# Kernel optimization log

Hardware: AMD Instinct MI355X
Metric: run time of the kernel (lower is better)

The kernel has to match this reference:

```python
import jax, jax.numpy as jnp
import numpy as np

LN_EPS = 1e-5
NEG_INF = -1e38


def wkv_scan(w, u, k, v):
    """Numerically-stable RWKV WKV recurrence (matches wkv_cuda forward).
    w: [C] (negative decay), u: [C] bonus, k/v: [B,T,C]. Returns y: [B,T,C]."""
    Bdim, T, C = k.shape

    def step(carry, kv_t):
        p, q, o = carry  # running num, den, log-scale, each [B,C]
        kt, vt = kv_t
        no = jnp.maximum(o, u + kt)
        A = jnp.exp(o - no)
        Bw = jnp.exp(u + kt - no)
        y = (A * p + Bw * vt) / (A * q + Bw)
        no2 = jnp.maximum(w + o, kt)
        A2 = jnp.exp(w + o - no2)
        B2 = jnp.exp(kt - no2)
        return (A2 * p + B2 * vt, A2 * q + B2, no2), y

    init = (jnp.zeros((Bdim, C), k.dtype), jnp.zeros((Bdim, C), k.dtype),
            jnp.full((Bdim, C), NEG_INF, k.dtype))
    kT = jnp.moveaxis(k, 1, 0)  # [T,B,C]
    vT = jnp.moveaxis(v, 1, 0)
    _, ys = jax.lax.scan(step, init, (kT, vT))
    return jnp.moveaxis(ys, 0, 1)  # [B,T,C]


def setup_inputs() -> dict:
    key = jax.random.key(0)
    ks = jax.random.split(key, 8)
    B, C, H, W = 16, 192, 56, 56
    s = 0.02
    x = jax.random.normal(ks[0], (B, C, H, W), jnp.float32)
    Wk = jax.random.normal(ks[1], (C, C), jnp.float32) * s
    Wv = jax.random.normal(ks[2], (C, C), jnp.float32) * s
    Wr = jax.random.normal(ks[3], (C, C), jnp.float32) * s
    Wo = jax.random.normal(ks[4], (C, C), jnp.float32) * s
    ln_g = jnp.ones((C,), jnp.float32)
    ln_b = jnp.zeros((C,), jnp.float32)
    w_decay = -6.0 + 0.1 * jax.random.normal(ks[5], (C,), jnp.float32)
    u = 0.1 * jax.random.normal(ks[6], (C,), jnp.float32)
    return {"x": x, "Wk": Wk, "Wv": Wv, "Wr": Wr, "Wo": Wo,
            "ln_g": ln_g, "ln_b": ln_b, "w_decay": w_decay, "u": u}


def reference(x, Wk, Wv, Wr, Wo, ln_g, ln_b, w_decay, u):
    B, C, H, W = x.shape
    xs = jnp.transpose(x.reshape(B, C, H * W), (0, 2, 1))  # [B,T,C]
    k = jnp.einsum('btc,dc->btd', xs, Wk)
    v = jnp.einsum('btc,dc->btd', xs, Wv)
    r = jnp.einsum('btc,dc->btd', xs, Wr)
    real_w = -jnp.exp(w_decay)
    x_fwd = wkv_scan(real_w, u, k, v)
    x_bwd = jnp.flip(wkv_scan(real_w, u, jnp.flip(k, 1), jnp.flip(v, 1)), 1)
    x_bi = 0.5 * (x_fwd + x_bwd)
    h = jax.nn.sigmoid(r) * x_bi
    mu = jnp.mean(h, axis=-1, keepdims=True)
    var = jnp.var(h, axis=-1, keepdims=True)
    h = (h - mu) * jax.lax.rsqrt(var + LN_EPS) * ln_g + ln_b
    out = jnp.einsum('btc,dc->btd', h, Wo)  # dropout is identity at eval
    return jnp.transpose(out, (0, 2, 1)).reshape(B, C, H, W)
```

## Files before the change

### kernel.cpp

```cpp
#include <hip/hip_runtime.h>

#define BB 16
#define CC 192
#define TPIX 3136
#define NCH 49
#define CHL 64
#define NNELE ((size_t)BB * TPIX * CC)
#define NSTATE ((size_t)2 * BB * NCH * CC)
#define WCH (CC * CC)

typedef __attribute__((ext_vector_type(8))) short bf16x8;
typedef __attribute__((ext_vector_type(4))) short bf16x4;
typedef __attribute__((ext_vector_type(4))) float f32x4;
typedef __attribute__((ext_vector_type(16))) float f32x16;

__device__ __forceinline__ unsigned short f2bf(float f) {
    union { float f; unsigned u; } v; v.f = f;
    unsigned r = v.u + 0x7FFFu + ((v.u >> 16) & 1u);
    return (unsigned short)(r >> 16);
}
__device__ __forceinline__ float bf2f(unsigned short h) {
    union { unsigned u; float f; } v; v.u = ((unsigned)h) << 16;
    return v.f;
}


__global__ __launch_bounds__(256) void wcvt_frag(
    const float* __restrict__ Wk, const float* __restrict__ Wv,
    const float* __restrict__ Wr, const float* __restrict__ Wo,
    unsigned short* __restrict__ wfrag)
{
    const int id = blockIdx.x * 256 + threadIdx.x;
    const int m = id / 4608;
    const int r = id % 4608;
    const int tile = r >> 6;
    const int lane = r & 63;
    const int dr = tile / 12, tk = tile % 12;
    const int d = dr * 32 + (lane & 31);
    const int c = tk * 16 + (lane >> 5) * 8;
    const float* W = (m == 0) ? Wk : (m == 1) ? Wv : (m == 2) ? Wr : Wo;
    const float4 a = *(const float4*)&W[d * CC + c];
    const float4 b = *(const float4*)&W[d * CC + c + 4];
    bf16x8 o;
    o[0] = (short)f2bf(a.x); o[1] = (short)f2bf(a.y);
    o[2] = (short)f2bf(a.z); o[3] = (short)f2bf(a.w);
    o[4] = (short)f2bf(b.x); o[5] = (short)f2bf(b.y);
    o[6] = (short)f2bf(b.z); o[7] = (short)f2bf(b.w);
    *(bf16x8*)&wfrag[(size_t)m * WCH + (size_t)tile * 512 + lane * 8] = o;
}

__global__ __launch_bounds__(256) void xcvt_frag(
    const float* __restrict__ x, unsigned short* __restrict__ xfrag)
{
    const int t0 = blockIdx.x * 32;
    const int b  = blockIdx.y;
    __shared__ float ls[CC][33];
    const int tid = threadIdx.x;
#pragma unroll
    for (int it = 0; it < 6; ++it) {
        const int c  = it * 32 + (tid >> 3);
        const int t4 = (tid & 7) * 4;
        *(float4*)&ls[c][t4] =
            *(const float4*)&x[((size_t)b * CC + c) * TPIX + t0 + t4];
    }
    __syncthreads();
    const size_t tbase = ((size_t)(b * TPIX + t0) >> 5) * 12;
#pragma unroll
    for (int it = 0; it < 3; ++it) {
        const int id = it * 256 + tid;
        const int tk = id >> 6;
        const int lane = id & 63;
        const int r32 = lane & 31;
        const int c0 = tk * 16 + (lane >> 5) * 8;
        bf16x8 o;
#pragma unroll
        for (int e = 0; e < 8; ++e)
            o[e] = (short)f2bf(ls[c0 + e][r32]);
        *(bf16x8*)&xfrag[(tbase + tk) * 512 + lane * 8] = o;
    }
}

__global__ __launch_bounds__(512) void proj_mfma32(
    const unsigned short* __restrict__ xfrag,
    const unsigned short* __restrict__ wfrag,
    unsigned short* __restrict__ kbf, unsigned short* __restrict__ vbf,
    unsigned short* __restrict__ rbf)
{
    __shared__ unsigned short wlds[WCH];
    const int tid  = threadIdx.x;
    const int lane = tid & 63;
    const int wv   = tid >> 6;
    const int tw   = wv >> 1;
    const int dwav = wv & 1;
    const int l31  = lane & 31;
    const int kh   = lane >> 5;
    const int m    = blockIdx.z;

    const unsigned short* wm = wfrag + (size_t)m * WCH;
#pragma unroll
    for (int it = 0; it < 9; ++it) {
        const int off = (it * 512 + tid) * 8;
        *(bf16x8*)&wlds[off] = *(const bf16x8*)&wm[off];
    }
    __syncthreads();

    const size_t row0 = (size_t)blockIdx.x * 128 + tw * 32;
    const size_t xtb  = (row0 >> 5) * 12;

    f32x16 acc[3];
#pragma unroll
    for (int nn = 0; nn < 3; ++nn)
#pragma unroll
        for (int e = 0; e < 16; ++e) acc[nn][e] = 0.f;

    bf16x8 xf = *(const bf16x8*)&xfrag[xtb * 512 + lane * 8];
#pragma unroll
    for (int ks = 0; ks < 12; ++ks) {
        bf16x8 nxf;
        if (ks < 11)
            nxf = *(const bf16x8*)&xfrag[(xtb + ks + 1) * 512 + lane * 8];
        bf16x8 wf[3];
#pragma unroll
        for (int nn = 0; nn < 3; ++nn)
            wf[nn] = *(const bf16x8*)&wlds[((dwav * 3 + nn) * 12 + ks) * 512 + lane * 8];
#pragma unroll
        for (int nn = 0; nn < 3; ++nn)
            acc[nn] = __builtin_amdgcn_mfma_f32_32x32x16_bf16(
                xf, wf[nn], acc[nn], 0, 0, 0);
        if (ks < 11) xf = nxf;
    }

    unsigned short* om = (m == 0) ? kbf : (m == 1) ? vbf : rbf;
#pragma unroll
    for (int nn = 0; nn < 3; ++nn) {
        const int d = dwav * 96 + nn * 32 + l31;
#pragma unroll
        for (int q = 0; q < 16; ++q) {
            const int t = (q & 3) + 8 * (q >> 2) + 4 * kh;
            om[(row0 + t) * CC + d] = f2bf(acc[nn][q]);
        }
    }
}

__global__ __launch_bounds__(512) void outproj_mfma32(
    const unsigned short* __restrict__ hfrag,
    const unsigned short* __restrict__ wo,
    float* __restrict__ out)
{
    __shared__ unsigned short wlds[WCH];
    const int tid  = threadIdx.x;
    const int lane = tid & 63;
    const int wv   = tid >> 6;
    const int tw   = wv >> 1;
    const int dwav = wv & 1;
    const int l31  = lane & 31;
    const int kh   = lane >> 5;

#pragma unroll
    for (int it = 0; it < 9; ++it) {
        const int off = (it * 512 + tid) * 8;
        *(bf16x8*)&wlds[off] = *(const bf16x8*)&wo[off];
    }
    __syncthreads();

    const size_t row0 = (size_t)blockIdx.x * 128 + tw * 32;
    const size_t htb  = (row0 >> 5) * 12;

    f32x16 acc[3];
#pragma unroll
    for (int nn = 0; nn < 3; ++nn)
#pragma unroll
        for (int e = 0; e < 16; ++e) acc[nn][e] = 0.f;

    bf16x8 hf = *(const bf16x8*)&hfrag[htb * 512 + lane * 8];
#pragma unroll
    for (int ks = 0; ks < 12; ++ks) {
        bf16x8 nhf;
        if (ks < 11)
            nhf = *(const bf16x8*)&hfrag[(htb + ks + 1) * 512 + lane * 8];
        bf16x8 wf[3];
#pragma unroll
        for (int nn = 0; nn < 3; ++nn)
            wf[nn] = *(const bf16x8*)&wlds[((dwav * 3 + nn) * 12 + ks) * 512 + lane * 8];
#pragma unroll
        for (int nn = 0; nn < 3; ++nn)
            acc[nn] = __builtin_amdgcn_mfma_f32_32x32x16_bf16(
                hf, wf[nn], acc[nn], 0, 0, 0);
        if (ks < 11) hf = nhf;
    }

#pragma unroll
    for (int nn = 0; nn < 3; ++nn) {
        const int d = dwav * 96 + nn * 32 + l31;
#pragma unroll
        for (int q2 = 0; q2 < 4; ++q2) {
            const size_t grow = row0 + 4 * kh + 8 * q2;
            const int b  = (int)(grow / TPIX);
            const int tl = (int)(grow % TPIX);
            f32x4 v4 = {acc[nn][q2 * 4 + 0], acc[nn][q2 * 4 + 1],
                        acc[nn][q2 * 4 + 2], acc[nn][q2 * 4 + 3]};
            *(f32x4*)&out[((size_t)b * CC + d) * TPIX + tl] = v4;
        }
    }
}

__global__ __launch_bounds__(256) void wkv_chunk_kernel(
    const unsigned short* __restrict__ kb, const unsigned short* __restrict__ vb,
    const float* __restrict__ wdec,
    float* __restrict__ sp, float* __restrict__ sq, float* __restrict__ so)
{
    const int gid = blockIdx.x * 256 + threadIdx.x;
    const int c  = gid % CC;
    const int r  = gid / CC;
    const int ch = r % NCH;
    const int r2 = r / NCH;
    const int b  = r2 % BB;
    const int dir = r2 / BB;

    const float w = -__expf(wdec[c]);
    const int tstart = dir ? (TPIX - 1 - ch * CHL) : (ch * CHL);
    const long stride = dir ? -(long)CC : (long)CC;
    long idx = ((long)b * TPIX + tstart) * CC + c;

    float p = 0.f, q = 0.f, o = -1e38f;
#pragma unroll 4
    for (int j = 0; j < CHL; ++j) {
        const float kt = bf2f(kb[idx]), vt = bf2f(vb[idx]);
        const float wo  = w + o;
        const float no2 = fmaxf(wo, kt);
        const float A2  = __expf(wo - no2);
        const float B2  = __expf(kt - no2);
        p = A2 * p + B2 * vt;
        q = A2 * q + B2;
        o = no2;
        idx += stride;
    }
    sp[gid] = p; sq[gid] = q; so[gid] = o;
}

__global__ __launch_bounds__(256) void wkv_prefix_kernel(
    float* __restrict__ sp, float* __restrict__ sq, float* __restrict__ so,
    const float* __restrict__ wdec)
{
    const int tid = blockIdx.x * 256 + threadIdx.x;
    if (tid >= 2 * BB * CC) return;
    const int c = tid % CC;
    const int g = tid / CC;
    const float w  = -__expf(wdec[c]);
    const float wL = w * CHL;

    float P = 0.f, Q = 0.f, O = -1e38f;
    size_t idx = (size_t)g * NCH * CC + c;
    for (int ch = 0; ch < NCH; ++ch) {
        const float pl = sp[idx], ql = sq[idx], ol = so[idx];
        sp[idx] = P; sq[idx] = Q; so[idx] = O;
        const float Ow = O + wL;
        const float no = fmaxf(Ow, ol);
        const float A  = __expf(Ow - no);
        const float Bf = __expf(ol - no);
        P = A * P + Bf * pl;
        Q = A * Q + Bf * ql;
        O = no;
        idx += CC;
    }
}

__global__ __launch_bounds__(192) void wkv_emit_ln(
    const unsigned short* __restrict__ kb, const unsigned short* __restrict__ vb,
    const unsigned short* __restrict__ rbf,
    const float* __restrict__ wdec, const float* __restrict__ ubias,
    const float* __restrict__ sp, const float* __restrict__ sq,
    const float* __restrict__ so,
    const float* __restrict__ gamma, const float* __restrict__ beta,
    unsigned short* __restrict__ hfrag)
{
    __shared__ float ylds[CHL][CC + 1];
    __shared__ float red[2][3][CHL];
    const int c  = threadIdx.x;
    const int ch = blockIdx.x;
    const int b  = blockIdx.y;
    const float w = -__expf(wdec[c]);
    const float u = ubias[c];
    const long rowbase = (long)b * TPIX + (long)ch * CHL;

    {
        const int gid = (b * NCH + ch) * CC + c;
        float p = sp[gid], q = sq[gid], o = so[gid];
        long idx = rowbase * CC + c;
        for (int j = 0; j < CHL; ++j) {
            const float kt = bf2f(kb[idx]), vt = bf2f(vb[idx]);
            const float uk  = u + kt;
            const float no  = fmaxf(o, uk);
            const float A   = __expf(o - no);
            const float Bw  = __expf(uk - no);
            ylds[j][c] = 0.5f * __fdividef(A * p + Bw * vt, A * q + Bw);
            const float wo  = w + o;
            const float no2 = fmaxf(wo, kt);
            const float A2  = __expf(wo - no2);
            const float B2  = __expf(kt - no2);
            p = A2 * p + B2 * vt;
            q = A2 * q + B2;
            o = no2;
            idx += CC;
        }
    }
    {
        const int gid = ((BB + b) * NCH + (NCH - 1 - ch)) * CC + c;
        float p = sp[gid], q = sq[gid], o = so[gid];
        long idx = (rowbase + CHL - 1) * CC + c;
        for (int j = 0; j < CHL; ++j) {
            const float kt = bf2f(kb[idx]), vt = bf2f(vb[idx]);
            const float uk  = u + kt;
            const float no  = fmaxf(o, uk);
            const float A   = __expf(o - no);
            const float Bw  = __expf(uk - no);
            ylds[CHL - 1 - j][c] += 0.5f * __fdividef(A * p + Bw * vt, A * q + Bw);
            const float wo  = w + o;
            const float no2 = fmaxf(wo, kt);
            const float A2  = __expf(wo - no2);
            const float B2  = __expf(kt - no2);
            p = A2 * p + B2 * vt;
            q = A2 * q + B2;
            o = no2;
            idx -= CC;
        }
    }
    {
        long idx = rowbase * CC + c;
        for (int j = 0; j < CHL; ++j) {
            const float rv = bf2f(rbf[idx]);
            ylds[j][c] *= __frcp_rn(1.f + __expf(-rv));
            idx += CC;
        }
    }
    __syncthreads();
    {
        const int rr = threadIdx.x & 63;
        const int g  = threadIdx.x >> 6;
        float s = 0.f, s2 = 0.f;
#pragma unroll 8
        for (int i = 0; i < 64; ++i) {
            const float v = ylds[rr][g * 64 + i];
            s += v; s2 += v * v;
        }
        red[0][g][rr] = s; red[1][g][rr] = s2;
    }
    __syncthreads();
    const float gm = gamma[c], bt = beta[c];
    for (int j = 0; j < CHL; ++j) {
        const float s  = red[0][0][j] + red[0][1][j] + red[0][2][j];
        const float s2 = red[1][0][j] + red[1][1][j] + red[1][2][j];
        const float mu   = s * (1.f / CC);
        const float var  = s2 * (1.f / CC) - mu * mu;
        const float rstd = rsqrtf(var + 1e-5f);
        const float hval = (ylds[j][c] - mu) * rstd * gm + bt;
        const size_t row = (size_t)rowbase + j;
        const size_t off = ((row >> 5) * 12 + (c >> 4)) * 512 +
                           ((row & 31) + ((c >> 3) & 1) * 32) * 8 + (c & 7);
        hfrag[off] = f2bf(hval);
    }
}

extern "C" void kernel_launch(void* const* d_in, const int* in_sizes, int n_in,
                              void* d_out, int out_size, void* d_ws, size_t ws_size,
                              hipStream_t stream)
{
    const float* x    = (const float*)d_in[0];
    const float* Wk   = (const float*)d_in[1];
    const float* Wv   = (const float*)d_in[2];
    const float* Wr   = (const float*)d_in[3];
    const float* Wo   = (const float*)d_in[4];
    const float* ln_g = (const float*)d_in[5];
    const float* ln_b = (const float*)d_in[6];
    const float* wdec = (const float*)d_in[7];
    const float* u    = (const float*)d_in[8];

    unsigned short* kbf   = (unsigned short*)d_ws;
    unsigned short* vbf   = kbf + NNELE;
    unsigned short* rbf   = vbf + NNELE;
    unsigned short* xfrag = rbf + NNELE;
    unsigned short* wfrag = xfrag + NNELE;
    unsigned short* hfrag = wfrag + 4 * WCH;
    float* sp = (float*)xfrag;
    float* sq = sp + NSTATE;
    float* so = sq + NSTATE;
    float* out = (float*)d_out;

    wcvt_frag<<<72, 256, 0, stream>>>(Wk, Wv, Wr, Wo, wfrag);
    xcvt_frag<<<dim3(TPIX / 32, BB), 256, 0, stream>>>(x, xfrag);

    proj_mfma32<<<dim3((BB * TPIX) / 128, 1, 3), 512, 0, stream>>>(
        xfrag, wfrag, kbf, vbf, rbf);

    const int nth = (int)NSTATE;
    wkv_chunk_kernel<<<nth / 256, 256, 0, stream>>>(kbf, vbf, wdec, sp, sq, so);
    wkv_prefix_kernel<<<(2 * BB * CC + 255) / 256, 256, 0, stream>>>(sp, sq, so, wdec);

    wkv_emit_ln<<<dim3(NCH, BB), 192, 0, stream>>>(
        kbf, vbf, rbf, wdec, u, sp, sq, so, ln_g, ln_b, hfrag);

    outproj_mfma32<<<(BB * TPIX) / 128, 512, 0, stream>>>(hfrag, wfrag + 3 * WCH, out);
}
```

Before: 158.5 us.

## Run forward and backward WKV emit scans concurrently in 384-thread blocks

The emit+LayerNorm kernel previously had each of 192 threads run the forward scan and then the backward scan serially over the 64-step chunk. Now blocks have 384 threads, and the two halves run the forward and backward scans in parallel, merging results into shared memory with LDS atomicAdd after zero-initialising the buffer. The sigmoid gating, row reduction and output stage are split across both halves. This halves the serial dependency chain per block, at the cost of atomic LDS traffic, an extra zero-init pass and barrier, and higher register and thread pressure per block.

```diff
diff --git a/kernel.cpp b/kernel.cpp
--- a/kernel.cpp
+++ b/kernel.cpp
@@ -265,7 +265,7 @@
     }
 }
 
-__global__ __launch_bounds__(192) void wkv_emit_ln(
+__global__ __launch_bounds__(384) void wkv_emit_ln(
     const unsigned short* __restrict__ kb, const unsigned short* __restrict__ vb,
     const unsigned short* __restrict__ rbf,
     const float* __restrict__ wdec, const float* __restrict__ ubias,
@@ -275,25 +275,37 @@
     unsigned short* __restrict__ hfrag)
 {
     __shared__ float ylds[CHL][CC + 1];
-    __shared__ float red[2][3][CHL];
-    const int c  = threadIdx.x;
-    const int ch = blockIdx.x;
-    const int b  = blockIdx.y;
+    __shared__ float red[2][6][CHL];
+    const int tid = threadIdx.x;
+    const int c   = tid % CC;
+    const int grp = tid / CC;
+    const int ch  = blockIdx.x;
+    const int b   = blockIdx.y;
     const float w = -__expf(wdec[c]);
     const float u = ubias[c];
     const long rowbase = (long)b * TPIX + (long)ch * CHL;
 
     {
-        const int gid = (b * NCH + ch) * CC + c;
+        float* yf = &ylds[0][0];
+        for (int i = tid; i < CHL * (CC + 1); i += 384) yf[i] = 0.f;
+    }
+    __syncthreads();
+
+    {
+        const int gid = grp ? (((BB + b) * NCH + (NCH - 1 - ch)) * CC + c)
+                            : ((b * NCH + ch) * CC + c);
         float p = sp[gid], q = sq[gid], o = so[gid];
-        long idx = rowbase * CC + c;
+        long idx = grp ? ((rowbase + CHL - 1) * CC + c) : (rowbase * CC + c);
+        const long stride = grp ? -(long)CC : (long)CC;
         for (int j = 0; j < CHL; ++j) {
             const float kt = bf2f(kb[idx]), vt = bf2f(vb[idx]);
             const float uk  = u + kt;
             const float no  = fmaxf(o, uk);
             const float A   = __expf(o - no);
             const float Bw  = __expf(uk - no);
-            ylds[j][c] = 0.5f * __fdividef(A * p + Bw * vt, A * q + Bw);
+            const int row = grp ? (CHL - 1 - j) : j;
+            atomicAdd(&ylds[row][c],
+                      0.5f * __fdividef(A * p + Bw * vt, A * q + Bw));
             const float wo  = w + o;
             const float no2 = fmaxf(wo, kt);
             const float A2  = __expf(wo - no2);
@@ -301,55 +313,41 @@
             p = A2 * p + B2 * vt;
             q = A2 * q + B2;
             o = no2;
-            idx += CC;
+            idx += stride;
         }
     }
+    __syncthreads();
+
     {
-        const int gid = ((BB + b) * NCH + (NCH - 1 - ch)) * CC + c;
-        float p = sp[gid], q = sq[gid], o = so[gid];
-        long idx = (rowbase + CHL - 1) * CC + c;
-        for (int j = 0; j < CHL; ++j) {
-            const float kt = bf2f(kb[idx]), vt = bf2f(vb[idx]);
-            const float uk  = u + kt;
-            const float no  = fmaxf(o, uk);
-            const float A   = __expf(o - no);
-            const float Bw  = __expf(uk - no);
-            ylds[CHL - 1 - j][c] += 0.5f * __fdividef(A * p + Bw * vt, A * q + Bw);
-            const float wo  = w + o;
-            const float no2 = fmaxf(wo, kt);
-            const float A2  = __expf(wo - no2);
-            const float B2  = __expf(kt - no2);
-            p = A2 * p + B2 * vt;
-            q = A2 * q + B2;
-            o = no2;
-            idx -= CC;
-        }
-    }
-    {
-        long idx = rowbase * CC + c;
-        for (int j = 0; j < CHL; ++j) {
+        const int j0 = grp * 32;
+        long idx = (rowbase + j0) * CC + c;
+        for (int j = j0; j < j0 + 32; ++j) {
             const float rv = bf2f(rbf[idx]);
             ylds[j][c] *= __frcp_rn(1.f + __expf(-rv));
             idx += CC;
         }
     }
     __syncthreads();
+
     {
-        const int rr = threadIdx.x & 63;
-        const int g  = threadIdx.x >> 6;
+        const int rr = tid & 63;
+        const int g  = tid >> 6;
         float s = 0.f, s2 = 0.f;
 #pragma unroll 8
-        for (int i = 0; i < 64; ++i) {
-            const float v = ylds[rr][g * 64 + i];
+        for (int i = 0; i < 32; ++i) {
+            const float v = ylds[rr][g * 32 + i];
             s += v; s2 += v * v;
         }
         red[0][g][rr] = s; red[1][g][rr] = s2;
     }
     __syncthreads();
+
     const float gm = gamma[c], bt = beta[c];
-    for (int j = 0; j < CHL; ++j) {
-        const float s  = red[0][0][j] + red[0][1][j] + red[0][2][j];
-        const float s2 = red[1][0][j] + red[1][1][j] + red[1][2][j];
+    const int j0 = grp * 32;
+    for (int j = j0; j < j0 + 32; ++j) {
+        float s = 0.f, s2 = 0.f;
+#pragma unroll
+        for (int g = 0; g < 6; ++g) { s += red[0][g][j]; s2 += red[1][g][j]; }
         const float mu   = s * (1.f / CC);
         const float var  = s2 * (1.f / CC) - mu * mu;
         const float rstd = rsqrtf(var + 1e-5f);
@@ -396,7 +394,7 @@
     wkv_chunk_kernel<<<nth / 256, 256, 0, stream>>>(kbf, vbf, wdec, sp, sq, so);
     wkv_prefix_kernel<<<(2 * BB * CC + 255) / 256, 256, 0, stream>>>(sp, sq, so, wdec);
 
-    wkv_emit_ln<<<dim3(NCH, BB), 192, 0, stream>>>(
+    wkv_emit_ln<<<dim3(NCH, BB), 384, 0, stream>>>(
         kbf, vbf, rbf, wdec, u, sp, sq, so, ln_g, ln_b, hfrag);
 
     outproj_mfma32<<<(BB * TPIX) / 128, 512, 0, stream>>>(hfrag, wfrag + 3 * WCH, out);
```

After: 222.1 us. 1.4x slower.
